# Kernel tuning notes

Measured on AMD Instinct MI355X. Metric: run time of the kernel, lower is better.

Reference implementation:

```python
import jax, jax.numpy as jnp
import numpy as np

LN_EPS = 1e-5

def _layer_norm(x):
    mu = jnp.mean(x, axis=-1, keepdims=True)
    var = jnp.var(x, axis=-1, keepdims=True)
    return (x - mu) / jnp.sqrt(var + LN_EPS)


def setup_inputs() -> dict:
    key = jax.random.key(0)
    ks = jax.random.split(key, 3)
    B, C, H, W = 8, 384, 48, 48
    x = jax.random.normal(ks[0], (B, C, H, W), dtype=jnp.float32)
    # torch Linear default init ~ U(-1/sqrt(fan_in), 1/sqrt(fan_in)); scaled normal is fine for a reference
    W1 = jax.random.normal(ks[1], (3 * C, C), dtype=jnp.float32) / np.sqrt(C)
    b1 = jnp.zeros((3 * C,), dtype=jnp.float32)
    W2 = jax.random.normal(ks[2], (C, C), dtype=jnp.float32) / np.sqrt(C)
    b2 = jnp.zeros((C,), dtype=jnp.float32)
    return {"x": x, "W1": W1, "b1": b1, "W2": W2, "b2": b2}


def reference(x, W1, b1, W2, b2):
    num_heads = 6
    B, C, H, W = x.shape
    N = H * W
    d = C // num_heads
    # [B,C,H,W] -> [B,N,C]
    t = x.reshape(B, C, N).transpose(0, 2, 1)
    t_norm = _layer_norm(t)
    qkv = t_norm @ W1.T + b1                      # [B,N,3C]
    q, k, v = jnp.split(qkv, 3, axis=-1)
    q = q.reshape(B, N, num_heads, d).transpose(0, 2, 1, 3)  # [B,h,N,d]
    k = k.reshape(B, N, num_heads, d).transpose(0, 2, 1, 3)
    v = v.reshape(B, N, num_heads, d).transpose(0, 2, 1, 3)
    att = jnp.einsum('bhnd,bhmd->bhnm', q, k) / jnp.sqrt(jnp.float32(d))
    att = jax.nn.softmax(att, axis=-1)            # dropout_prob = 0.0 -> identity
    o = jnp.einsum('bhnm,bhmd->bhnd', att, v)     # [B,h,N,d]
    o = o.transpose(0, 2, 1, 3).reshape(B, N, C)
    o = o @ W2.T + b2
    out = (o + t_norm).transpose(0, 2, 1).reshape(B, C, H, W)
    return out
```

## Files before the change

kernel.cpp:

```cpp
#include <hip/hip_runtime.h>
#include <cstdint>

#define DEVI __device__ __forceinline__

typedef unsigned short u16;
typedef __attribute__((ext_vector_type(4))) u16 u16x4;
typedef __attribute__((ext_vector_type(2))) unsigned int u32x2;
typedef __attribute__((ext_vector_type(2))) float f32x2;
typedef __attribute__((ext_vector_type(4))) float f32x4;
typedef __attribute__((ext_vector_type(8))) float f32x8;
typedef __attribute__((ext_vector_type(16))) float f32x16;
typedef __attribute__((ext_vector_type(8))) __bf16 bf16x8;

constexpr int kB = 8, kC = 384, kN = 2304, kNH = 6, kD = 64;
constexpr int kM = kB * kN;
constexpr int k3C = 3 * kC;
constexpr int kNT = kN / 64;
constexpr int kKS = kC / 32;

DEVI float bf2f(u16 u) {
  union { unsigned int u; float f; } v; v.u = ((unsigned int)u) << 16; return v.f;
}
DEVI u16 f2bf(float f) {
  union { float f; unsigned int u; } v; v.f = f;
  return (u16)((v.u + 0x7fffu + ((v.u >> 16) & 1u)) >> 16);
}
DEVI void gload16(const void* g, void* l) {
  __builtin_amdgcn_global_load_lds(
      (__attribute__((address_space(1))) void*)const_cast<void*>(g),
      (__attribute__((address_space(3))) void*)l, 16, 0, 0);
}
DEVI bf16x8 ldg8(const u16* p) { return *reinterpret_cast<const bf16x8*>(p); }

DEVI float fexp2(float x) {
#if __has_builtin(__builtin_amdgcn_exp2f)
  return __builtin_amdgcn_exp2f(x);
#else
  return exp2f(x);
#endif
}

DEVI unsigned cvtpk(float lo, float hi) {
  unsigned r;
  asm("v_cvt_pk_bf16_f32 %0, %1, %2" : "=v"(r) : "v"(lo), "v"(hi));
  return r;
}
DEVI void plswap(unsigned& a, unsigned& b) {
#if __has_builtin(__builtin_amdgcn_permlane32_swap)
  auto rr = __builtin_amdgcn_permlane32_swap(a, b, false, false);
  a = rr[0]; b = rr[1];
#else
  unsigned ax = __shfl_xor(a, 32, 64), bx = __shfl_xor(b, 32, 64);
  int hi = (threadIdx.x & 63) >> 5;
  unsigned r0 = hi ? bx : a;
  unsigned r1 = hi ? b : ax;
  a = r0; b = r1;
#endif
}

DEVI bf16x8 ldsw(const u16* base, int row, int cb) {
  return *reinterpret_cast<const bf16x8*>(
      (const char*)base + row * 128 + (cb ^ ((row & 7) << 4)));
}

__global__ __launch_bounds__(256) void ln_kernel(const float* __restrict__ x,
                                                 u16* __restrict__ tn) {
  const int b = blockIdx.x & 7;
  const int n0 = (blockIdx.x >> 3) * 64;
  const int t = threadIdx.x;
  const int tni = t & 63, tc = t >> 6;
  const float* xb = x + (size_t)b * kC * kN;

  float sum = 0.f, ssq = 0.f;
  for (int c = tc; c < kC; c += 4) {
    float v = xb[(size_t)c * kN + n0 + tni];
    sum += v; ssq += v * v;
  }
  __shared__ float red[8][64];
  red[tc][tni] = sum; red[tc + 4][tni] = ssq;
  __syncthreads();
  __shared__ float s_mu[64], s_rs[64];
  if (t < 64) {
    float s = red[0][t] + red[1][t] + red[2][t] + red[3][t];
    float q = red[4][t] + red[5][t] + red[6][t] + red[7][t];
    float mu = s * (1.f / kC);
    float var = q * (1.f / kC) - mu * mu;
    s_mu[t] = mu; s_rs[t] = rsqrtf(var + 1e-5f);
  }
  __syncthreads();
  __shared__ float tile[64][65];
  for (int c0 = 0; c0 < kC; c0 += 64) {
#pragma unroll
    for (int kk = 0; kk < 16; ++kk) {
      int cl = tc * 16 + kk;
      tile[tni][cl] = xb[(size_t)(c0 + cl) * kN + n0 + tni];
    }
    __syncthreads();
#pragma unroll
    for (int kk = 0; kk < 16; ++kk) {
      int nl = tc * 16 + kk;
      float v = (tile[nl][tni] - s_mu[nl]) * s_rs[nl];
      tn[((size_t)b * kN + n0 + nl) * kC + c0 + tni] = f2bf(v);
    }
    __syncthreads();
  }
}

__global__ __launch_bounds__(256) void cast_w(const float* __restrict__ W1, const float* __restrict__ W2,
                                              u16* __restrict__ w1b, u16* __restrict__ w2b) {
  int i = blockIdx.x * 256 + threadIdx.x;
  if (i < k3C * kC) w1b[i] = f2bf(W1[i]);
  if (i < kC * kC)  w2b[i] = f2bf(W2[i]);
}

DEVI int swzg(int r, int sl) { return (sl ^ ((r >> 1) & 3)) * 8; }

#define GSTAGE(dstLds, gbase, kt)                                        \
  {                                                                      \
    _Pragma("unroll")                                                    \
    for (int c = 0; c < 2; ++c) {                                        \
      int i = c * 256 + t;                                               \
      int r = i >> 2, sl = i & 3;                                        \
      gload16((gbase) + (size_t)r * kC + (kt) + swzg(r, sl),             \
              (dstLds) + (c * 256 + (t & 192)) * 8);                     \
    }                                                                    \
  }

DEVI void gemm_core(const u16* __restrict__ A, const u16* __restrict__ Bm,
                    f32x4 acc[4][4], u16* lA, u16* lB) {
  const int t = threadIdx.x;
  const int lane = t & 63;
  const int w = t >> 6, wr = w >> 1, wc = w & 1;
  const int lr = lane & 15, lg = lane >> 4;

  GSTAGE(lA, A, 0)
  GSTAGE(lB, Bm, 0)

  int cur = 0;
#pragma unroll 3
  for (int s = 0; s < kKS; ++s) {
    const u16* cA = lA + cur * 4096;
    const u16* cB = lB + cur * 4096;
    const int nxt = (cur == 2) ? 0 : cur + 1;
    if (s + 1 < kKS) {
      GSTAGE(lA + nxt * 4096, A, (s + 1) * 32)
      GSTAGE(lB + nxt * 4096, Bm, (s + 1) * 32)
      asm volatile("s_waitcnt vmcnt(4)" ::: "memory");
    } else {
      asm volatile("s_waitcnt vmcnt(0)" ::: "memory");
    }
    __builtin_amdgcn_s_barrier();
    __builtin_amdgcn_sched_barrier(0);

    bf16x8 af[4], bfr[4];
#pragma unroll
    for (int f = 0; f < 4; ++f) {
      int row = wr * 64 + f * 16 + lr;
      af[f] = ldg8(&cA[row * 32 + swzg(row, lg)]);
    }
#pragma unroll
    for (int f = 0; f < 4; ++f) {
      int row = wc * 64 + f * 16 + lr;
      bfr[f] = ldg8(&cB[row * 32 + swzg(row, lg)]);
    }
    __builtin_amdgcn_s_setprio(1);
#pragma unroll
    for (int fm = 0; fm < 4; ++fm)
#pragma unroll
      for (int fn = 0; fn < 4; ++fn)
        acc[fm][fn] = __builtin_amdgcn_mfma_f32_16x16x32_bf16(af[fm], bfr[fn], acc[fm][fn], 0, 0, 0);
    __builtin_amdgcn_s_setprio(0);
    cur = nxt;
  }
}

__global__ __launch_bounds__(256) void qkv_kernel(const u16* __restrict__ tn, const u16* __restrict__ w1b,
                                                  const float* __restrict__ b1,
                                                  u16* __restrict__ q, u16* __restrict__ kbuf,
                                                  u16* __restrict__ vTout) {
  __shared__ u16 lAs[3 * 4096], lBs[3 * 4096];
  const int wg = blockIdx.x;
  const int xcd = wg & 7, idx = wg >> 3;
  const int m0 = (xcd * 18 + idx / 9) * 128;
  const int o0 = (idx % 9) * 128;
  f32x4 acc[4][4] = {};
  gemm_core(tn + (size_t)m0 * kC, w1b + (size_t)o0 * kC, acc, lAs, lBs);

  const int t = threadIdx.x, lane = t & 63, w = t >> 6;
  const int wr = w >> 1, wc = w & 1, lr = lane & 15, lg = lane >> 4;
  const float kQScale = 0.125f * 1.44269504088896f;
  const int bb = m0 / kN;
  const int nb0 = m0 % kN;
#pragma unroll
  for (int fm = 0; fm < 4; ++fm)
#pragma unroll
    for (int fn = 0; fn < 4; ++fn) {
      int o = o0 + wc * 64 + fn * 16 + lr;
      float bias = b1[o];
      if (o < kC) {
        int h = o >> 6, dd = o & 63;
#pragma unroll
        for (int r = 0; r < 4; ++r) {
          int n = nb0 + wr * 64 + fm * 16 + lg * 4 + r;
          q[(((size_t)bb * kNH + h) * kN + n) * kD + dd] = f2bf((acc[fm][fn][r] + bias) * kQScale);
        }
      } else if (o < 2 * kC) {
        int o2 = o - kC, h = o2 >> 6, dd = o2 & 63;
#pragma unroll
        for (int r = 0; r < 4; ++r) {
          int n = nb0 + wr * 64 + fm * 16 + lg * 4 + r;
          kbuf[(((size_t)bb * kNH + h) * kN + n) * kD + dd] = f2bf(acc[fm][fn][r] + bias);
        }
      } else {
        int o2 = o - 2 * kC, h = o2 >> 6, dd = o2 & 63;
        int n4 = nb0 + wr * 64 + fm * 16 + lg * 4;
        u16x4 pk;
#pragma unroll
        for (int r = 0; r < 4; ++r) pk[r] = f2bf(acc[fm][fn][r] + bias);
        *reinterpret_cast<u16x4*>(&vTout[(((size_t)bb * kNH + h) * kD + dd) * kN + n4]) = pk;
      }
    }
}

#define PV_STEP(SV, OFF, KS)                                                          \
  {                                                                                   \
    unsigned a0 = cvtpk(SV[OFF + 0], SV[OFF + 1]);                                    \
    unsigned a1 = cvtpk(SV[OFF + 2], SV[OFF + 3]);                                    \
    unsigned a2 = cvtpk(SV[OFF + 4], SV[OFF + 5]);                                    \
    unsigned a3 = cvtpk(SV[OFF + 6], SV[OFF + 7]);                                    \
    plswap(a0, a2); plswap(a1, a3);                                                   \
    union { unsigned wds[4]; bf16x8 v; } pu;                                          \
    pu.wds[0] = a0; pu.wds[1] = a1; pu.wds[2] = a2; pu.wds[3] = a3;                   \
    bf16x8 vf0 = ldsw(vL, ql, (KS) * 32 + hi * 16);                                   \
    bf16x8 vf1 = ldsw(vL, 32 + ql, (KS) * 32 + hi * 16);                              \
    o0 = __builtin_amdgcn_mfma_f32_32x32x16_bf16(vf0, pu.v, o0, 0, 0, 0);             \
    o1 = __builtin_amdgcn_mfma_f32_32x32x16_bf16(vf1, pu.v, o1, 0, 0, 0);             \
    o2 = __builtin_amdgcn_mfma_f32_32x32x16_bf16(onesf, pu.v, o2, 0, 0, 0);           \
  }

#define STAGE(dstLds, gbase, gstride)                                                 \
  {                                                                                   \
    _Pragma("unroll")                                                                 \
    for (int c = 0; c < 2; ++c) {                                                     \
      int i = c * 256 + t;                                                            \
      int r = i >> 3;                                                                 \
      int cb = ((i & 7) * 16) ^ ((r & 7) << 4);                                       \
      gload16((gbase) + (size_t)r * (gstride) + cb,                                   \
              (dstLds) + c * 2048 + (t & 192) * 8);                                   \
    }                                                                                 \
  }

__global__ __launch_bounds__(256) void attn_kernel(const u16* __restrict__ qg, const u16* __restrict__ kg,
                                                   const u16* __restrict__ vT, u16* __restrict__ obuf) {
  const int wg = blockIdx.x;
  const int xcd = wg & 7, idx = wg >> 3;
  const int bh = xcd * 6 + idx / 18;
  const int qt = idx % 18;
  const int b = bh / kNH, h = bh % kNH;
  const int t = threadIdx.x, lane = t & 63, w = t >> 6;
  const int q0w = qt * 128 + w * 32;
  const int ql = lane & 31;
  const int hi = lane >> 5;
  const u16* qb  = qg + (size_t)bh * kN * kD;
  const char* kbB = (const char*)(kg + (size_t)bh * kN * kD);
  const char* vbT = (const char*)(vT + (size_t)bh * kD * kN);

  __shared__ u16 kLds[3 * 4096];
  __shared__ u16 vLds[3 * 4096];

  bf16x8 qf[4];
#pragma unroll
  for (int ds = 0; ds < 4; ++ds)
    qf[ds] = ldg8(&qb[(size_t)(q0w + ql) * kD + ds * 16 + hi * 8]);

  bf16x8 onesf;
#pragma unroll
  for (int j = 0; j < 8; ++j) onesf[j] = (__bf16)1.0f;

  f32x16 o0 = {}, o1 = {}, o2 = {};

  STAGE(kLds, kbB, 128)
  STAGE(vLds, vbT, kN * 2)

  int cur = 0;
  for (int ti = 0; ti < kNT; ++ti) {
    const u16* kL = kLds + cur * 4096;
    const u16* vL = vLds + cur * 4096;
    const int nxt = (cur == 2) ? 0 : cur + 1;
    if (ti + 1 < kNT) {
      const char* kNext = kbB + (size_t)(ti + 1) * 64 * 128;
      const char* vNext = vbT + (size_t)(ti + 1) * 128;
      STAGE(kLds + nxt * 4096, kNext, 128)
      STAGE(vLds + nxt * 4096, vNext, kN * 2)
      asm volatile("s_waitcnt vmcnt(4)" ::: "memory");
    } else {
      asm volatile("s_waitcnt vmcnt(0)" ::: "memory");
    }
    __builtin_amdgcn_s_barrier();
    __builtin_amdgcn_sched_barrier(0);

    f32x16 s0 = {}, s1 = {};
#pragma unroll
    for (int ds = 0; ds < 4; ++ds) {
      bf16x8 kf0 = ldsw(kL, ql, ds * 32 + hi * 16);
      bf16x8 kf1 = ldsw(kL, 32 + ql, ds * 32 + hi * 16);
      s0 = __builtin_amdgcn_mfma_f32_32x32x16_bf16(kf0, qf[ds], s0, 0, 0, 0);
      s1 = __builtin_amdgcn_mfma_f32_32x32x16_bf16(kf1, qf[ds], s1, 0, 0, 0);
    }

#pragma unroll
    for (int r = 0; r < 16; ++r) {
      s0[r] = fexp2(s0[r]);
      s1[r] = fexp2(s1[r]);
    }

    PV_STEP(s0, 0, 0)
    PV_STEP(s0, 8, 1)
    PV_STEP(s1, 0, 2)
    PV_STEP(s1, 8, 3)

    cur = nxt;
  }

  const float inv = 1.f / o2[0];
  {
    const size_t row = ((size_t)b * kN + q0w + ql) * kC + h * 64;
#pragma unroll
    for (int g = 0; g < 4; ++g) {
      u32x2 pk;
      pk.x = cvtpk(o0[g * 4 + 0] * inv, o0[g * 4 + 1] * inv);
      pk.y = cvtpk(o0[g * 4 + 2] * inv, o0[g * 4 + 3] * inv);
      *reinterpret_cast<u32x2*>(&obuf[row + g * 8 + 4 * hi]) = pk;
    }
#pragma unroll
    for (int g = 0; g < 4; ++g) {
      u32x2 pk;
      pk.x = cvtpk(o1[g * 4 + 0] * inv, o1[g * 4 + 1] * inv);
      pk.y = cvtpk(o1[g * 4 + 2] * inv, o1[g * 4 + 3] * inv);
      *reinterpret_cast<u32x2*>(&obuf[row + 32 + g * 8 + 4 * hi]) = pk;
    }
  }
}

__global__ __launch_bounds__(256) void proj_kernel(const u16* __restrict__ obuf, const u16* __restrict__ w2b,
                                                   const float* __restrict__ b2, const u16* __restrict__ tn,
                                                   float* __restrict__ out) {
  __shared__ u16 lAs[3 * 4096], lBs[3 * 4096];
  const int wg = blockIdx.x;
  const int xcd = wg & 7, idx = wg >> 3;
  const int bn = xcd * 18 + idx / 3;
  const int b = bn / 18;
  const int n0 = (bn % 18) * 128;
  const int c0 = (idx % 3) * 128;
  f32x4 acc[4][4] = {};
  gemm_core(w2b + (size_t)c0 * kC, obuf + ((size_t)b * kN + n0) * kC, acc, lAs, lBs);

  const int t = threadIdx.x, lane = t & 63, w = t >> 6;
  const int wr = w >> 1, wc = w & 1, lr = lane & 15, lg = lane >> 4;
#pragma unroll
  for (int fm = 0; fm < 4; ++fm)
#pragma unroll
    for (int fn = 0; fn < 4; ++fn) {
      int n = n0 + wc * 64 + fn * 16 + lr;
#pragma unroll
      for (int r = 0; r < 4; ++r) {
        int c = c0 + wr * 64 + fm * 16 + lg * 4 + r;
        float val = acc[fm][fn][r] + b2[c] + bf2f(tn[((size_t)b * kN + n) * kC + c]);
        out[((size_t)b * kC + c) * kN + n] = val;
      }
    }
}

extern "C" void kernel_launch(void* const* d_in, const int* in_sizes, int n_in,
                              void* d_out, int out_size, void* d_ws, size_t ws_size,
                              hipStream_t stream) {
  const float* x  = (const float*)d_in[0];
  const float* W1 = (const float*)d_in[1];
  const float* b1 = (const float*)d_in[2];
  const float* W2 = (const float*)d_in[3];
  const float* b2 = (const float*)d_in[4];
  float* out = (float*)d_out;

  const size_t nBNC = (size_t)kM * kC;
  u16* tn  = (u16*)d_ws;
  u16* qb  = tn  + nBNC;
  u16* kb  = qb  + nBNC;
  u16* vb  = kb  + nBNC;
  u16* vT  = vb  + nBNC;
  u16* w1b = vT  + nBNC;
  u16* w2b = w1b + (size_t)k3C * kC;
  u16* obuf = vb;

  ln_kernel<<<dim3(kB * (kN / 64)), dim3(256), 0, stream>>>(x, tn);
  cast_w<<<dim3((k3C * kC + 255) / 256), dim3(256), 0, stream>>>(W1, W2, w1b, w2b);
  qkv_kernel<<<dim3(kM / 128 * (k3C / 128)), dim3(256), 0, stream>>>(tn, w1b, b1, qb, kb, vT);
  attn_kernel<<<dim3((kN / 128) * kB * kNH), dim3(256), 0, stream>>>(qb, kb, vT, obuf);
  proj_kernel<<<dim3((kN / 128) * (kC / 128) * kB), dim3(256), 0, stream>>>(obuf, w2b, b2, tn, out);
}
```

Measured before the change: 186.2 us.

## Stage Q/K epilogue through LDS and widen attention blocks to 512 threads

The QKV GEMM epilogue for the Q and K tiles now writes the accumulators into a padded shared-memory tile. It then stores them as contiguous 16-byte vectors instead of scattered 2-byte stores, and the V-transpose path is split into its own branch. The attention kernel moves to 256 query rows per block with 8 waves, so each K/V tile staged in LDS is shared by twice as many query rows. Each thread now issues one load per stage, and the wait count is adjusted to match. This halves the number of attention blocks and doubles the threads per block, which changes occupancy and may affect load balance across CUs.

```diff
diff --git a/kernel.cpp b/kernel.cpp
--- a/kernel.cpp
+++ b/kernel.cpp
@@ -178,41 +178,29 @@
                                                   const float* __restrict__ b1,
                                                   u16* __restrict__ q, u16* __restrict__ kbuf,
                                                   u16* __restrict__ vTout) {
-  __shared__ u16 lAs[3 * 4096], lBs[3 * 4096];
+  __shared__ u16 shmem[6 * 4096];
   const int wg = blockIdx.x;
   const int xcd = wg & 7, idx = wg >> 3;
   const int m0 = (xcd * 18 + idx / 9) * 128;
   const int o0 = (idx % 9) * 128;
   f32x4 acc[4][4] = {};
-  gemm_core(tn + (size_t)m0 * kC, w1b + (size_t)o0 * kC, acc, lAs, lBs);
+  gemm_core(tn + (size_t)m0 * kC, w1b + (size_t)o0 * kC, acc, shmem, shmem + 3 * 4096);
 
   const int t = threadIdx.x, lane = t & 63, w = t >> 6;
   const int wr = w >> 1, wc = w & 1, lr = lane & 15, lg = lane >> 4;
   const float kQScale = 0.125f * 1.44269504088896f;
   const int bb = m0 / kN;
   const int nb0 = m0 % kN;
-#pragma unroll
-  for (int fm = 0; fm < 4; ++fm)
+  const int ot = o0 >> 7;
+
+  if (ot >= 6) {
 #pragma unroll
     for (int fn = 0; fn < 4; ++fn) {
-      int o = o0 + wc * 64 + fn * 16 + lr;
-      float bias = b1[o];
-      if (o < kC) {
-        int h = o >> 6, dd = o & 63;
-#pragma unroll
-        for (int r = 0; r < 4; ++r) {
-          int n = nb0 + wr * 64 + fm * 16 + lg * 4 + r;
-          q[(((size_t)bb * kNH + h) * kN + n) * kD + dd] = f2bf((acc[fm][fn][r] + bias) * kQScale);
-        }
-      } else if (o < 2 * kC) {
-        int o2 = o - kC, h = o2 >> 6, dd = o2 & 63;
-#pragma unroll
-        for (int r = 0; r < 4; ++r) {
-          int n = nb0 + wr * 64 + fm * 16 + lg * 4 + r;
-          kbuf[(((size_t)bb * kNH + h) * kN + n) * kD + dd] = f2bf(acc[fm][fn][r] + bias);
-        }
-      } else {
-        int o2 = o - 2 * kC, h = o2 >> 6, dd = o2 & 63;
+      int ol = o0 - 2 * kC + wc * 64 + fn * 16 + lr;
+      float bias = b1[2 * kC + ol];
+      int h = ol >> 6, dd = ol & 63;
+#pragma unroll
+      for (int fm = 0; fm < 4; ++fm) {
         int n4 = nb0 + wr * 64 + fm * 16 + lg * 4;
         u16x4 pk;
 #pragma unroll
@@ -220,6 +208,34 @@
         *reinterpret_cast<u16x4*>(&vTout[(((size_t)bb * kNH + h) * kD + dd) * kN + n4]) = pk;
       }
     }
+  } else {
+    __syncthreads();
+    const float scale = (ot < 3) ? kQScale : 1.0f;
+#pragma unroll
+    for (int fn = 0; fn < 4; ++fn) {
+      int col = wc * 64 + fn * 16 + lr;
+      float bias = b1[o0 + col];
+#pragma unroll
+      for (int fm = 0; fm < 4; ++fm)
+#pragma unroll
+        for (int r = 0; r < 4; ++r) {
+          int row = wr * 64 + fm * 16 + lg * 4 + r;
+          shmem[row * 132 + col] = f2bf((acc[fm][fn][r] + bias) * scale);
+        }
+    }
+    __syncthreads();
+    u16* outp = (ot < 3) ? q : kbuf;
+    const int h0 = (o0 - (ot < 3 ? 0 : kC)) >> 6;
+#pragma unroll
+    for (int it = 0; it < 8; ++it) {
+      int ci = it * 256 + t;
+      int row = ci >> 4, ck = ci & 15;
+      int c = ck * 8;
+      int h = h0 + (c >> 6), dd = c & 63;
+      *reinterpret_cast<bf16x8*>(&outp[(((size_t)bb * kNH + h) * kN + nb0 + row) * kD + dd]) =
+          *reinterpret_cast<const bf16x8*>(&shmem[row * 132 + c]);
+    }
+  }
 }
 
 #define PV_STEP(SV, OFF, KS)                                                          \
@@ -240,25 +256,21 @@
 
 #define STAGE(dstLds, gbase, gstride)                                                 \
   {                                                                                   \
-    _Pragma("unroll")                                                                 \
-    for (int c = 0; c < 2; ++c) {                                                     \
-      int i = c * 256 + t;                                                            \
-      int r = i >> 3;                                                                 \
-      int cb = ((i & 7) * 16) ^ ((r & 7) << 4);                                       \
-      gload16((gbase) + (size_t)r * (gstride) + cb,                                   \
-              (dstLds) + c * 2048 + (t & 192) * 8);                                   \
-    }                                                                                 \
-  }
-
-__global__ __launch_bounds__(256) void attn_kernel(const u16* __restrict__ qg, const u16* __restrict__ kg,
+    int r_ = t >> 3;                                                                  \
+    int cb_ = ((t & 7) * 16) ^ ((r_ & 7) << 4);                                       \
+    gload16((gbase) + (size_t)r_ * (gstride) + cb_,                                   \
+            (dstLds) + (t & 448) * 8);                                                \
+  }
+
+__global__ __launch_bounds__(512) void attn_kernel(const u16* __restrict__ qg, const u16* __restrict__ kg,
                                                    const u16* __restrict__ vT, u16* __restrict__ obuf) {
   const int wg = blockIdx.x;
   const int xcd = wg & 7, idx = wg >> 3;
-  const int bh = xcd * 6 + idx / 18;
-  const int qt = idx % 18;
+  const int bh = xcd * 6 + idx / 9;
+  const int qt = idx % 9;
   const int b = bh / kNH, h = bh % kNH;
   const int t = threadIdx.x, lane = t & 63, w = t >> 6;
-  const int q0w = qt * 128 + w * 32;
+  const int q0w = qt * 256 + w * 32;
   const int ql = lane & 31;
   const int hi = lane >> 5;
   const u16* qb  = qg + (size_t)bh * kN * kD;
@@ -292,7 +304,7 @@
       const char* vNext = vbT + (size_t)(ti + 1) * 128;
       STAGE(kLds + nxt * 4096, kNext, 128)
       STAGE(vLds + nxt * 4096, vNext, kN * 2)
-      asm volatile("s_waitcnt vmcnt(4)" ::: "memory");
+      asm volatile("s_waitcnt vmcnt(2)" ::: "memory");
     } else {
       asm volatile("s_waitcnt vmcnt(0)" ::: "memory");
     }
@@ -394,6 +406,6 @@
   ln_kernel<<<dim3(kB * (kN / 64)), dim3(256), 0, stream>>>(x, tn);
   cast_w<<<dim3((k3C * kC + 255) / 256), dim3(256), 0, stream>>>(W1, W2, w1b, w2b);
   qkv_kernel<<<dim3(kM / 128 * (k3C / 128)), dim3(256), 0, stream>>>(tn, w1b, b1, qb, kb, vT);
-  attn_kernel<<<dim3((kN / 128) * kB * kNH), dim3(256), 0, stream>>>(qb, kb, vT, obuf);
+  attn_kernel<<<dim3((kN / 256) * kB * kNH), dim3(512), 0, stream>>>(qb, kb, vT, obuf);
   proj_kernel<<<dim3((kN / 128) * (kC / 128) * kB), dim3(256), 0, stream>>>(obuf, w2b, b2, tn, out);
 }
```

Result: faster. 168.7 us (-9.4%).
